# Kernel tuning notes

Hardware: AMD Instinct MI355X
Metric: run time of the kernel (lower is better)

The kernel has to match this reference:

```python
import jax, jax.numpy as jnp
import numpy as np

N = 50000   # nodes
E = 800000  # edges (avg degree 16)
G = 32      # graphs in batch
IN = 128; HID = 64; H = 2; C = 16
NEG_SLOPE = 0.2
BN_EPS = 1e-5


def setup_inputs() -> dict:
    key = jax.random.key(0)
    ks = jax.random.split(key, 16)
    def rn(k, shape, scale=0.1):
        return jax.random.normal(k, shape, jnp.float32) * scale
    return {
        "feat": jax.random.normal(ks[0], (N, IN), jnp.float32),
        "W0": rn(ks[1], (IN, H * HID)),
        "attn0": rn(ks[2], (H, HID)),
        "W1": rn(ks[3], (H * HID, H * HID)),
        "attn1": rn(ks[4], (H, HID)),
        "W2": rn(ks[5], (H * HID, H * HID)),
        "attn2": rn(ks[6], (H, HID)),
        "Wf": rn(ks[7], (H * HID, H * C)),
        "attnf": rn(ks[8], (H, C)),
        "mlp_w1": rn(ks[9], (C, C)),
        "mlp_gamma": jnp.ones((C,), jnp.float32),
        "mlp_beta": jnp.zeros((C,), jnp.float32),
        "mlp_w2": rn(ks[10], (C, C)),
        "src": jax.random.randint(ks[11], (E,), 0, N, jnp.int32),
        "dst": jax.random.randint(ks[12], (E,), 0, N, jnp.int32),
        "node_graph": jnp.sort(jax.random.randint(ks[13], (N,), 0, G, jnp.int32)),
        "num_graphs": G,
    }


def gatv2_layer(h, src, dst, W, attn, act):
    """DGL GATv2Conv with share_weights=True, bias=False, residual=False."""
    n = h.shape[0]
    nh, d = attn.shape
    z = (h @ W).reshape(n, nh, d)                      # [N,H,D]
    zs = z[src]                                        # [E,H,D] gather (src)
    e = jax.nn.leaky_relu(zs + z[dst], NEG_SLOPE)      # [E,H,D]
    score = jnp.einsum('ehd,hd->eh', e, attn)          # [E,H]
    # edge softmax over incoming edges of dst (shift-invariant max trick)
    m = jax.lax.stop_gradient(jax.ops.segment_max(score, dst, num_segments=n))
    a = jnp.exp(score - m[dst])
    denom = jax.ops.segment_sum(a, dst, num_segments=n)[dst]
    alpha = a / jnp.where(denom == 0, 1.0, denom)      # [E,H]
    out = jax.ops.segment_sum(alpha[..., None] * zs, dst, num_segments=n)  # [N,H,D]
    return act(out) if act is not None else out


def reference(feat, W0, attn0, W1, attn1, W2, attn2, Wf, attnf,
              mlp_w1, mlp_gamma, mlp_beta, mlp_w2,
              src, dst, node_graph, num_graphs):
    relu = jax.nn.relu
    n = feat.shape[0]
    h = gatv2_layer(feat, src, dst, W0, attn0, relu).reshape(n, -1)
    h = gatv2_layer(h, src, dst, W1, attn1, relu).reshape(n, -1)
    h = gatv2_layer(h, src, dst, W2, attn2, relu).reshape(n, -1)
    logits = gatv2_layer(h, src, dst, Wf, attnf, None).mean(axis=1)  # [N,C]
    pooled = jax.ops.segment_sum(logits, node_graph, num_segments=num_graphs)  # [G,C]
    # MLP: relu(batchnorm(lin0(x))) -> lin1 (training-mode batch stats, biased var)
    h1 = pooled @ mlp_w1
    mu = h1.mean(axis=0)
    var = h1.var(axis=0)
    h1 = (h1 - mu) / jnp.sqrt(var + BN_EPS) * mlp_gamma + mlp_beta
    out = relu(h1) @ mlp_w2
    return jax.nn.log_softmax(out, axis=-1)
```

## Files before the change

### kernel.cpp

```cpp
#include <hip/hip_runtime.h>
#include <hip/hip_bf16.h>
#include <hip/hip_fp16.h>
#include <math.h>

#define NN 50000
#define EE 800000
#define GG 32
#define HD 64
#define NHEAD 2
#define CCLS 16
#define NEG_SLOPE 0.2f
#define BN_EPS 1e-5f
#define LOG2E 1.4426950408889634f
#define STRIDE 64
#define CURB 6250
#define BUCKCAP 110000
#define SLICES 392
#define LCAP 192

typedef unsigned int u32;
typedef unsigned short u16;
typedef unsigned long long u64;
typedef _Float16 hv2 __attribute__((ext_vector_type(2)));
typedef __fp16   cv2 __attribute__((ext_vector_type(2)));

__device__ __forceinline__ hv2 bch2(u32 u) { union { u32 u; hv2 h; } c; c.u = u; return c.h; }
__device__ __forceinline__ u32 bcu32(hv2 h) { union { hv2 h; u32 u; } c; c.h = h; return c.u; }
__device__ __forceinline__ u32 pkrtz(float a, float b) {
    cv2 r = __builtin_amdgcn_cvt_pkrtz(a, b);
    union { cv2 h; u32 u; } c; c.h = r; return c.u;
}
__device__ __forceinline__ hv2 h2max(hv2 a, hv2 b) {
    return __builtin_elementwise_max(a, b);
}
__device__ __forceinline__ float fdot2(hv2 a, hv2 b, float c) {
#if __has_builtin(__builtin_amdgcn_fdot2)
    union { hv2 h; cv2 c2; } ua, ub;
    ua.h = a; ub.h = b;
    return __builtin_amdgcn_fdot2(ua.c2, ub.c2, c, false);
#else
    return fmaf((float)a[0], (float)b[0], fmaf((float)a[1], (float)b[1], c));
#endif
}
__device__ __forceinline__ int curidx(int d) { return (d & 7) * CURB + (d >> 3); }


__global__ __launch_bounds__(256) void bucket_kernel(const int* __restrict__ src,
                                                     const int* __restrict__ dst,
                                                     int* __restrict__ bcur,
                                                     u32* __restrict__ buckets,
                                                     int* __restrict__ cursor,
                                                     u16* __restrict__ csr_src) {
    __shared__ int cnt[8], base[8];
    __shared__ u32 buf[8 * LCAP];
    int t = threadIdx.x;
    int lane = t & 63;
    if (t < 8) cnt[t] = 0;
    __syncthreads();
    #pragma unroll
    for (int q = 0; q < 4; q++) {
        int e = blockIdx.x * 1024 + q * 256 + t;
        bool v = e < EE;
        int d = v ? dst[e] : 0;
        int s = v ? src[e] : 0;
        int mybucket = v ? (d & 7) : 8;
        u32 pkv = ((u32)d << 16) | (u32)s;
        #pragma unroll
        for (int b = 0; b < 8; b++) {
            u64 m = __ballot(mybucket == b);
            if (m == 0ull) continue;
            int leader = __ffsll((long long)m) - 1;
            int bs = 0;
            if (lane == leader) bs = atomicAdd(&cnt[b], __popcll(m));
            bs = __shfl(bs, leader, 64);
            if (mybucket == b) {
                int pos = bs + __popcll(m & ((1ull << lane) - 1ull));
                if (pos < LCAP) {
                    buf[b * LCAP + pos] = pkv;
                } else {
                    int p = atomicAdd(&cursor[curidx(d)], 1);
                    csr_src[d * STRIDE + p] = (u16)s;
                }
            }
        }
    }
    __syncthreads();
    if (t < 8) {
        int c = min(cnt[t], LCAP);
        cnt[t] = c;
        base[t] = atomicAdd(&bcur[t], c);
    }
    __syncthreads();
    #pragma unroll
    for (int b = 0; b < 8; b++) {
        int c = cnt[b], bs = base[b];
        for (int i = t; i < c; i += 256)
            buckets[b * BUCKCAP + bs + i] = buf[b * LCAP + i];
    }
}


__global__ __launch_bounds__(256) void scatter2_kernel(const u32* __restrict__ buckets,
                                                       const int* __restrict__ bcur,
                                                       int* __restrict__ cursor,
                                                       u16* __restrict__ csr_src) {
    int b = blockIdx.x & 7;
    int slice = blockIdx.x >> 3;
    int cnt = bcur[b];
    const u32* bp = buckets + b * BUCKCAP;
    for (int idx = slice * 256 + threadIdx.x; idx < cnt; idx += SLICES * 256) {
        u32 pk = bp[idx];
        int d = pk >> 16;
        int s = pk & 0xffff;
        int p = atomicAdd(&cursor[b * CURB + (d >> 3)], 1);
        csr_src[d * STRIDE + p] = (u16)s;
    }
}


template<int KOUT, int RPT, bool F16IN>
__device__ __forceinline__ void gemm_body(const void* __restrict__ hv,
                                          const float* __restrict__ W,
                                          u32* __restrict__ z, int n, int blk) {
    constexpr int CT = KOUT / 8;
    constexpr int RT = 256 / CT;
    constexpr int BR = RT * RPT;
    constexpr int WSTR = (KOUT == 128) ? 140 : (KOUT + 4);
    __shared__ __align__(16) u32 WpD[64 * WSTR];
    __shared__ __align__(16) uint4 hsU4[BR * 17];
    int t = threadIdx.x;
    int row0 = blk * BR;

    for (int i = t; i < 64 * (KOUT / 4); i += 256) {
        int k2 = i / (KOUT / 4), cq = i % (KOUT / 4);
        float4 wa = ((const float4*)W)[(2 * k2) * (KOUT / 4) + cq];
        float4 wb = ((const float4*)W)[(2 * k2 + 1) * (KOUT / 4) + cq];
        uint4 d;
        d.x = pkrtz(wa.x, wb.x); d.y = pkrtz(wa.y, wb.y);
        d.z = pkrtz(wa.z, wb.z); d.w = pkrtz(wa.w, wb.w);
        *(uint4*)&WpD[k2 * WSTR + 4 * cq + ((cq >> 3) << 2)] = d;
    }
    for (int i = t; i < BR * 16; i += 256) {
        int r = i >> 4, c16 = i & 15;
        int gr = row0 + r;
        uint4 u = {0, 0, 0, 0};
        if (gr < n) {
            if (F16IN) {
                u = ((const uint4*)hv)[(size_t)gr * 16 + c16];
            } else {
                float4 f0 = ((const float4*)hv)[(size_t)gr * 32 + 2 * c16];
                float4 f1 = ((const float4*)hv)[(size_t)gr * 32 + 2 * c16 + 1];
                u.x = pkrtz(f0.x, f0.y); u.y = pkrtz(f0.z, f0.w);
                u.z = pkrtz(f1.x, f1.y); u.w = pkrtz(f1.z, f1.w);
            }
        }
        hsU4[r * 17 + c16] = u;
    }
    __syncthreads();

    int tc = t % CT, tr = t / CT;
    float acc[RPT][8];
    #pragma unroll
    for (int i = 0; i < RPT; i++)
        #pragma unroll
        for (int c = 0; c < 8; c++) acc[i][c] = 0.f;

    for (int kq = 0; kq < 16; kq++) {
        uint4 a4[RPT];
        #pragma unroll
        for (int i = 0; i < RPT; i++) a4[i] = hsU4[(tr * RPT + i) * 17 + kq];
        #pragma unroll
        for (int j = 0; j < 4; j++) {
            const u32* wrow = &WpD[(4 * kq + j) * WSTR + tc * 8 + ((tc >> 2) << 2)];
            uint4 wa = *(const uint4*)wrow;
            uint4 wb = *(const uint4*)(wrow + 4);
            u32 wd[8] = {wa.x, wa.y, wa.z, wa.w, wb.x, wb.y, wb.z, wb.w};
            #pragma unroll
            for (int i = 0; i < RPT; i++) {
                u32 av[4] = {a4[i].x, a4[i].y, a4[i].z, a4[i].w};
                hv2 a2 = bch2(av[j]);
                #pragma unroll
                for (int c = 0; c < 8; c++)
                    acc[i][c] = fdot2(a2, bch2(wd[c]), acc[i][c]);
            }
        }
    }
    #pragma unroll
    for (int i = 0; i < RPT; i++) {
        int gr = row0 + tr * RPT + i;
        if (gr < n) {
            uint4 p;
            p.x = pkrtz(acc[i][0], acc[i][1]);
            p.y = pkrtz(acc[i][2], acc[i][3]);
            p.z = pkrtz(acc[i][4], acc[i][5]);
            p.w = pkrtz(acc[i][6], acc[i][7]);
            ((uint4*)z)[(size_t)gr * (KOUT / 8) + tc] = p;
        }
    }
}

template<int KOUT, int RPT, bool F16IN>
__global__ __launch_bounds__(256) void gemm_kernel(const void* __restrict__ hv,
                                                   const float* __restrict__ W,
                                                   u32* __restrict__ z, int n) {
    gemm_body<KOUT, RPT, F16IN>(hv, W, z, n, blockIdx.x);
}

__global__ __launch_bounds__(256) void gemm0_kernel(const void* __restrict__ hv,
                                                    const float* __restrict__ W,
                                                    u32* __restrict__ z,
                                                    int* __restrict__ cursor,
                                                    float* __restrict__ pooled) {
    int gid = blockIdx.x * 256 + threadIdx.x;
    if (gid < NN + 8) cursor[gid] = 0;
    if (gid < GG * CCLS) pooled[gid] = 0.f;
    gemm_body<128, 4, false>(hv, W, z, NN, blockIdx.x);
}


__global__ __launch_bounds__(256) void edge_kernel(const u32* __restrict__ z,
                                                   const float* __restrict__ attn,
                                                   const int* __restrict__ cursor,
                                                   const u16* __restrict__ csr_src,
                                                   u32* __restrict__ out, int n) {
    int wave = blockIdx.x * 4 + (threadIdx.x >> 6);
    int lane = threadIdx.x & 63;
    if (wave >= n) return;
    int i = wave;
    int slot = lane >> 3;
    int q8 = lane & 7;
    const uint4* zr = (const uint4*)z;

    size_t rowi = (size_t)i * 16 + q8 * 2;
    uint4 zua = zr[rowi], zub = zr[rowi + 1];
    hv2 zd[8] = {bch2(zua.x), bch2(zua.y), bch2(zua.z), bch2(zua.w),
                 bch2(zub.x), bch2(zub.y), bch2(zub.z), bch2(zub.w)};
    const float4* af = (const float4*)attn;
    float4 a0 = af[q8 * 4 + 0], a1 = af[q8 * 4 + 1];
    float4 a2 = af[q8 * 4 + 2], a3 = af[q8 * 4 + 3];
    hv2 ah[8] = {bch2(pkrtz(a0.x * LOG2E, a0.y * LOG2E)),
                 bch2(pkrtz(a0.z * LOG2E, a0.w * LOG2E)),
                 bch2(pkrtz(a1.x * LOG2E, a1.y * LOG2E)),
                 bch2(pkrtz(a1.z * LOG2E, a1.w * LOG2E)),
                 bch2(pkrtz(a2.x * LOG2E, a2.y * LOG2E)),
                 bch2(pkrtz(a2.z * LOG2E, a2.w * LOG2E)),
                 bch2(pkrtz(a3.x * LOG2E, a3.y * LOG2E)),
                 bch2(pkrtz(a3.z * LOG2E, a3.w * LOG2E))};
    const hv2 slope2 = {(_Float16)NEG_SLOPE, (_Float16)NEG_SLOPE};

    int deg = cursor[curidx(i)];
    const u16* ep = csr_src + i * STRIDE;

    float s = 0.f;
    hv2 acch[8];
    #pragma unroll
    for (int j = 0; j < 8; j++) acch[j] = (hv2){(_Float16)0.f, (_Float16)0.f};

    bool valid = slot < deg;
    int sid = valid ? (int)ep[slot] : i;
    size_t rs = (size_t)sid * 16 + q8 * 2;
    uint4 sa = zr[rs], sb = zr[rs + 1];

    for (int k = 0; k < deg; k += 8) {
        bool more = (k + 8) < deg;
        bool v2 = (k + 8 + slot) < deg;
        uint4 na, nb;
        if (more) {
            int sid2 = v2 ? (int)ep[k + 8 + slot] : i;
            size_t rs2 = (size_t)sid2 * 16 + q8 * 2;
            na = zr[rs2]; nb = zr[rs2 + 1];
        }
        hv2 zs[8] = {bch2(sa.x), bch2(sa.y), bch2(sa.z), bch2(sa.w),
                     bch2(sb.x), bch2(sb.y), bch2(sb.z), bch2(sb.w)};
        float sc = 0.f;
        #pragma unroll
        for (int j = 0; j < 8; j++) {
            hv2 x = zs[j] + zd[j];
            x = h2max(x, x * slope2);
            sc = fdot2(x, ah[j], sc);
        }
        sc += __shfl_xor(sc, 2, 64);
        sc += __shfl_xor(sc, 1, 64);
        float p = valid ? exp2f(sc) : 0.f;
        s += p;
        hv2 p2 = bch2(pkrtz(p, p));
        #pragma unroll
        for (int j = 0; j < 8; j++) acch[j] = p2 * zs[j] + acch[j];
        sa = na; sb = nb; valid = v2;
    }

    #pragma unroll
    for (int off = 8; off <= 32; off <<= 1) {
        s += __shfl_xor(s, off, 64);
        #pragma unroll
        for (int j = 0; j < 8; j++) {
            u32 o = (u32)__shfl_xor((int)bcu32(acch[j]), off, 64);
            acch[j] = acch[j] + bch2(o);
        }
    }

    if (slot == 0) {
        float inv = s > 0.f ? 1.f / s : 0.f;
        hv2 inv2 = bch2(pkrtz(inv, inv));
        const hv2 zero2 = {(_Float16)0.f, (_Float16)0.f};
        uint4 pa, pb;
        pa.x = bcu32(h2max(acch[0] * inv2, zero2));
        pa.y = bcu32(h2max(acch[1] * inv2, zero2));
        pa.z = bcu32(h2max(acch[2] * inv2, zero2));
        pa.w = bcu32(h2max(acch[3] * inv2, zero2));
        pb.x = bcu32(h2max(acch[4] * inv2, zero2));
        pb.y = bcu32(h2max(acch[5] * inv2, zero2));
        pb.z = bcu32(h2max(acch[6] * inv2, zero2));
        pb.w = bcu32(h2max(acch[7] * inv2, zero2));
        ((uint4*)out)[rowi] = pa;
        ((uint4*)out)[rowi + 1] = pb;
    }
}


__global__ __launch_bounds__(256) void edge_final_kernel(const u32* __restrict__ z,
                                                         const float* __restrict__ attn,
                                                         const int* __restrict__ cursor,
                                                         const u16* __restrict__ csr_src,
                                                         const int* __restrict__ node_graph,
                                                         float* __restrict__ pooled, int n) {
    __shared__ float pl[GG * CCLS];
    for (int t = threadIdx.x; t < GG * CCLS; t += 256) pl[t] = 0.f;
    __syncthreads();

    int wave = blockIdx.x * 4 + (threadIdx.x >> 6);
    int lane = threadIdx.x & 63;
    int iv = wave * 2 + (lane >> 5);
    bool mine = iv < n;
    int i = mine ? iv : (n - 1);
    int hl = lane & 31;
    int j = hl >> 3;
    int d8 = hl & 7;
    const uint2* zr = (const uint2*)z;
    uint2 zu = zr[(size_t)i * 8 + d8];
    hv2 zd0 = bch2(zu.x), zd1 = bch2(zu.y);
    float4 av = ((const float4*)attn)[d8];
    hv2 ah0 = bch2(pkrtz(av.x * LOG2E, av.y * LOG2E));
    hv2 ah1 = bch2(pkrtz(av.z * LOG2E, av.w * LOG2E));
    const hv2 slope2 = {(_Float16)NEG_SLOPE, (_Float16)NEG_SLOPE};
    int deg = cursor[curidx(i)];
    const u16* ep = csr_src + i * STRIDE;

    float s = 0.f;
    float accf[4] = {0.f, 0.f, 0.f, 0.f};
    for (int k = 0; k < deg; k += 4) {
        int kk = k + j;
        bool valid = kk < deg;
        int sid = valid ? (int)ep[kk] : i;
        uint2 su = zr[(size_t)sid * 8 + d8];
        hv2 zs0 = bch2(su.x), zs1 = bch2(su.y);
        hv2 x;
        float sc = 0.f;
        x = zs0 + zd0; x = h2max(x, x * slope2); sc = fdot2(x, ah0, sc);
        x = zs1 + zd1; x = h2max(x, x * slope2); sc = fdot2(x, ah1, sc);
        sc += __shfl_xor(sc, 1, 64);
        sc += __shfl_xor(sc, 2, 64);
        float p = valid ? exp2f(sc) : 0.f;
        s += p;
        accf[0] = fmaf(p, (float)zs0[0], accf[0]);
        accf[1] = fmaf(p, (float)zs0[1], accf[1]);
        accf[2] = fmaf(p, (float)zs1[0], accf[2]);
        accf[3] = fmaf(p, (float)zs1[1], accf[3]);
    }
    #pragma unroll
    for (int off = 8; off <= 16; off <<= 1) {
        s += __shfl_xor(s, off, 64);
        #pragma unroll
        for (int jj = 0; jj < 4; jj++) accf[jj] += __shfl_xor(accf[jj], off, 64);
    }
    float inv = s > 0.f ? 1.f / s : 0.f;
    float4 o;
    o.x = accf[0] * inv; o.y = accf[1] * inv; o.z = accf[2] * inv; o.w = accf[3] * inv;
    o.x = 0.5f * (o.x + __shfl_xor(o.x, 4, 64));
    o.y = 0.5f * (o.y + __shfl_xor(o.y, 4, 64));
    o.z = 0.5f * (o.z + __shfl_xor(o.z, 4, 64));
    o.w = 0.5f * (o.w + __shfl_xor(o.w, 4, 64));
    if (mine && j == 0 && (hl & 4) == 0) {
        int g = node_graph[i];
        float* base = &pl[g * 16 + 4 * d8];
        atomicAdd(&base[0], o.x);
        atomicAdd(&base[1], o.y);
        atomicAdd(&base[2], o.z);
        atomicAdd(&base[3], o.w);
    }
    __syncthreads();
    for (int t = threadIdx.x; t < GG * CCLS; t += 256) {
        float v = pl[t];
        if (v != 0.f) atomicAdd(&pooled[t], v);
    }
}


__global__ __launch_bounds__(512) void mlp_kernel(const float* __restrict__ pooled,
                                                  const float* __restrict__ w1,
                                                  const float* __restrict__ gamma,
                                                  const float* __restrict__ beta,
                                                  const float* __restrict__ w2,
                                                  float* __restrict__ out) {
    __shared__ float P[GG * CCLS], H1[GG * CCLS], H2[GG * CCLS], O[GG * CCLS];
    __shared__ float mu[CCLS], rstd[CCLS], rowm[GG], rowl[GG];
    int t = threadIdx.x;
    int r = t >> 4, c = t & 15;
    if (t < GG * CCLS) P[t] = pooled[t];
    __syncthreads();
    if (t < GG * CCLS) {
        float s = 0.f;
        for (int k = 0; k < 16; k++) s += P[r * 16 + k] * w1[k * 16 + c];
        H1[t] = s;
    }
    __syncthreads();
    if (t < CCLS) {
        float s = 0.f;
        for (int rr = 0; rr < GG; rr++) s += H1[rr * 16 + t];
        float mn = s / GG;
        float s2 = 0.f;
        for (int rr = 0; rr < GG; rr++) { float d = H1[rr * 16 + t] - mn; s2 += d * d; }
        mu[t] = mn; rstd[t] = rsqrtf(s2 / GG + BN_EPS);
    }
    __syncthreads();
    if (t < GG * CCLS) {
        float v = (H1[t] - mu[c]) * rstd[c] * gamma[c] + beta[c];
        H2[t] = fmaxf(v, 0.f);
    }
    __syncthreads();
    if (t < GG * CCLS) {
        float s = 0.f;
        for (int k = 0; k < 16; k++) s += H2[r * 16 + k] * w2[k * 16 + c];
        O[t] = s;
    }
    __syncthreads();
    if (t < GG) {
        float mx = -INFINITY;
        for (int k = 0; k < 16; k++) mx = fmaxf(mx, O[t * 16 + k]);
        float l = 0.f;
        for (int k = 0; k < 16; k++) l += __expf(O[t * 16 + k] - mx);
        rowm[t] = mx; rowl[t] = logf(l);
    }
    __syncthreads();
    if (t < GG * CCLS) out[t] = O[t] - rowm[r] - rowl[r];
}


extern "C" void kernel_launch(void* const* d_in, const int* in_sizes, int n_in,
                              void* d_out, int out_size, void* d_ws, size_t ws_size,
                              hipStream_t stream) {
    const float* feat     = (const float*)d_in[0];
    const float* W0       = (const float*)d_in[1];
    const float* attn0    = (const float*)d_in[2];
    const float* W1       = (const float*)d_in[3];
    const float* attn1    = (const float*)d_in[4];
    const float* W2       = (const float*)d_in[5];
    const float* attn2    = (const float*)d_in[6];
    const float* Wf       = (const float*)d_in[7];
    const float* attnf    = (const float*)d_in[8];
    const float* mlp_w1   = (const float*)d_in[9];
    const float* mlp_g    = (const float*)d_in[10];
    const float* mlp_b    = (const float*)d_in[11];
    const float* mlp_w2   = (const float*)d_in[12];
    const int*   src      = (const int*)d_in[13];
    const int*   dst      = (const int*)d_in[14];
    const int*   ngraph   = (const int*)d_in[15];
    float* out = (float*)d_out;

    char* ws = (char*)d_ws;
    size_t off = 0;
    auto alloc = [&](size_t bytes) {
        void* p = ws + off;
        off = (off + bytes + 255) & ~(size_t)255;
        return p;
    };
    u32* z      = (u32*)alloc((size_t)NN * 64 * sizeof(u32));
    u32* hb0    = (u32*)alloc((size_t)NN * 64 * sizeof(u32));
    u32* hb1    = (u32*)alloc((size_t)NN * 64 * sizeof(u32));
    float* pooled = (float*)alloc(GG * CCLS * sizeof(float));
    int* cursor   = (int*)alloc((NN + 8) * sizeof(int));
    int* bcur     = cursor + NN;
    u16* csr_src  = (u16*)alloc((size_t)NN * STRIDE * sizeof(u16));
    u32* buckets  = (u32*)alloc((size_t)8 * BUCKCAP * sizeof(u32));

    int edge_grid = (NN + 3) / 4;
    int edgef_grid = (NN + 7) / 8;
    int gemm_grid = (NN + 63) / 64;
    int buck_grid = (EE + 1023) / 1024;

    gemm0_kernel<<<gemm_grid, 256, 0, stream>>>(feat, W0, z, cursor, pooled);
    bucket_kernel<<<buck_grid, 256, 0, stream>>>(src, dst, bcur, buckets, cursor, csr_src);
    scatter2_kernel<<<8 * SLICES, 256, 0, stream>>>(buckets, bcur, cursor, csr_src);
    edge_kernel<<<edge_grid, 256, 0, stream>>>(z, attn0, cursor, csr_src, hb0, NN);

    gemm_kernel<128, 4, true><<<gemm_grid, 256, 0, stream>>>(hb0, W1, z, NN);
    edge_kernel<<<edge_grid, 256, 0, stream>>>(z, attn1, cursor, csr_src, hb1, NN);

    gemm_kernel<128, 4, true><<<gemm_grid, 256, 0, stream>>>(hb1, W2, z, NN);
    edge_kernel<<<edge_grid, 256, 0, stream>>>(z, attn2, cursor, csr_src, hb0, NN);

    gemm_kernel<32, 1, true><<<gemm_grid, 256, 0, stream>>>(hb0, Wf, z, NN);
    edge_final_kernel<<<edgef_grid, 256, 0, stream>>>(z, attnf, cursor, csr_src,
                                                      ngraph, pooled, NN);

    mlp_kernel<<<1, 512, 0, stream>>>(pooled, mlp_w1, mlp_g, mlp_b, mlp_w2, out);
}
```

Measured before the change: 380.7 us.

## Co-schedule layer-0 GEMM with CSR scatter and fuse MLP into final edge kernel

Moves the layer-0 GEMM out of the first kernel into a combined launch whose blocks either run a K-chunked GEMM tile with a smaller LDS arena or scatter bucketed edges into the CSR, so the two independent jobs share the GPU at the same time. The first kernel is now a small zero-init kernel. The MLP head is folded into the last edge kernel through a last-block-done ticket counter, which removes one launch. The cost is an extra atomic per block and a serial tail in the final block, plus the GEMM reloading W chunks.

```diff
diff --git a/kernel.cpp b/kernel.cpp
--- a/kernel.cpp
+++ b/kernel.cpp
@@ -15,8 +15,13 @@
 #define STRIDE 64
 #define CURB 6250
 #define BUCKCAP 110000
-#define SLICES 392
 #define LCAP 192
+#define NCHUNK ((EE + 1023) / 1024)
+#define NTILE  ((NN + 63) / 64)
+#define G0B 784
+#define SCB 752
+#define NBF (G0B + SCB)
+#define SLC (SCB / 8)
 
 typedef unsigned int u32;
 typedef unsigned short u16;
@@ -43,6 +48,16 @@
 #endif
 }
 __device__ __forceinline__ int curidx(int d) { return (d & 7) * CURB + (d >> 3); }
+
+
+__global__ __launch_bounds__(256) void zero_kernel(int* __restrict__ cursor,
+                                                   float* __restrict__ pooled,
+                                                   int* __restrict__ done) {
+    int g = blockIdx.x * 256 + threadIdx.x;
+    for (int i = g; i < NN + 8; i += gridDim.x * 256) cursor[i] = 0;
+    if (g < GG * CCLS) pooled[g] = 0.f;
+    if (g == 0) *done = 0;
+}
 
 
 __global__ __launch_bounds__(256) void bucket_kernel(const int* __restrict__ src,
@@ -100,24 +115,6 @@
 }
 
 
-__global__ __launch_bounds__(256) void scatter2_kernel(const u32* __restrict__ buckets,
-                                                       const int* __restrict__ bcur,
-                                                       int* __restrict__ cursor,
-                                                       u16* __restrict__ csr_src) {
-    int b = blockIdx.x & 7;
-    int slice = blockIdx.x >> 3;
-    int cnt = bcur[b];
-    const u32* bp = buckets + b * BUCKCAP;
-    for (int idx = slice * 256 + threadIdx.x; idx < cnt; idx += SLICES * 256) {
-        u32 pk = bp[idx];
-        int d = pk >> 16;
-        int s = pk & 0xffff;
-        int p = atomicAdd(&cursor[b * CURB + (d >> 3)], 1);
-        csr_src[d * STRIDE + p] = (u16)s;
-    }
-}
-
-
 template<int KOUT, int RPT, bool F16IN>
 __device__ __forceinline__ void gemm_body(const void* __restrict__ hv,
                                           const float* __restrict__ W,
@@ -206,15 +203,113 @@
     gemm_body<KOUT, RPT, F16IN>(hv, W, z, n, blockIdx.x);
 }
 
-__global__ __launch_bounds__(256) void gemm0_kernel(const void* __restrict__ hv,
-                                                    const float* __restrict__ W,
-                                                    u32* __restrict__ z,
-                                                    int* __restrict__ cursor,
-                                                    float* __restrict__ pooled) {
-    int gid = blockIdx.x * 256 + threadIdx.x;
-    if (gid < NN + 8) cursor[gid] = 0;
-    if (gid < GG * CCLS) pooled[gid] = 0.f;
-    gemm_body<128, 4, false>(hv, W, z, NN, blockIdx.x);
+__device__ __forceinline__ void gemm_body_chunk(const float* __restrict__ hv,
+                                                const float* __restrict__ W,
+                                                u32* __restrict__ z, int n, int blk,
+                                                char* arena) {
+    constexpr int WSTR = 140;
+    constexpr int KC = 16;
+    u32* WpD = (u32*)arena;
+    uint4* hsU4 = (uint4*)(arena + 9216);
+    int t = threadIdx.x;
+    int row0 = blk * 64;
+
+    for (int i = t; i < 64 * 16; i += 256) {
+        int r = i >> 4, c16 = i & 15;
+        int gr = row0 + r;
+        uint4 u = {0, 0, 0, 0};
+        if (gr < n) {
+            float4 f0 = ((const float4*)hv)[(size_t)gr * 32 + 2 * c16];
+            float4 f1 = ((const float4*)hv)[(size_t)gr * 32 + 2 * c16 + 1];
+            u.x = pkrtz(f0.x, f0.y); u.y = pkrtz(f0.z, f0.w);
+            u.z = pkrtz(f1.x, f1.y); u.w = pkrtz(f1.z, f1.w);
+        }
+        hsU4[r * 17 + c16] = u;
+    }
+
+    int tc = t % 16, tr = t / 16;
+    float acc[4][8];
+    #pragma unroll
+    for (int i = 0; i < 4; i++)
+        #pragma unroll
+        for (int c = 0; c < 8; c++) acc[i][c] = 0.f;
+
+    for (int ch = 0; ch < 4; ch++) {
+        __syncthreads();
+        for (int i = t; i < KC * 32; i += 256) {
+            int k2l = i / 32, cq = i % 32;
+            int k2 = ch * KC + k2l;
+            float4 wa = ((const float4*)W)[(2 * k2) * 32 + cq];
+            float4 wb = ((const float4*)W)[(2 * k2 + 1) * 32 + cq];
+            uint4 d;
+            d.x = pkrtz(wa.x, wb.x); d.y = pkrtz(wa.y, wb.y);
+            d.z = pkrtz(wa.z, wb.z); d.w = pkrtz(wa.w, wb.w);
+            *(uint4*)&WpD[k2l * WSTR + 4 * cq + ((cq >> 3) << 2)] = d;
+        }
+        __syncthreads();
+        for (int kqq = 0; kqq < KC / 4; kqq++) {
+            int kq = ch * (KC / 4) + kqq;
+            uint4 a4[4];
+            #pragma unroll
+            for (int i = 0; i < 4; i++) a4[i] = hsU4[(tr * 4 + i) * 17 + kq];
+            #pragma unroll
+            for (int j = 0; j < 4; j++) {
+                const u32* wrow = &WpD[(4 * kqq + j) * WSTR + tc * 8 + ((tc >> 2) << 2)];
+                uint4 wa = *(const uint4*)wrow;
+                uint4 wb = *(const uint4*)(wrow + 4);
+                u32 wd[8] = {wa.x, wa.y, wa.z, wa.w, wb.x, wb.y, wb.z, wb.w};
+                #pragma unroll
+                for (int i = 0; i < 4; i++) {
+                    u32 av[4] = {a4[i].x, a4[i].y, a4[i].z, a4[i].w};
+                    hv2 a2 = bch2(av[j]);
+                    #pragma unroll
+                    for (int c = 0; c < 8; c++)
+                        acc[i][c] = fdot2(a2, bch2(wd[c]), acc[i][c]);
+                }
+            }
+        }
+    }
+    #pragma unroll
+    for (int i = 0; i < 4; i++) {
+        int gr = row0 + tr * 4 + i;
+        if (gr < n) {
+            uint4 p;
+            p.x = pkrtz(acc[i][0], acc[i][1]);
+            p.y = pkrtz(acc[i][2], acc[i][3]);
+            p.z = pkrtz(acc[i][4], acc[i][5]);
+            p.w = pkrtz(acc[i][6], acc[i][7]);
+            ((uint4*)z)[(size_t)gr * 16 + tc] = p;
+        }
+    }
+}
+
+
+__global__ __launch_bounds__(256, 6) void g0scat_kernel(const float* __restrict__ feat,
+                                                        const float* __restrict__ W0,
+                                                        u32* __restrict__ z,
+                                                        const u32* __restrict__ buckets,
+                                                        const int* __restrict__ bcur,
+                                                        int* __restrict__ cursor,
+                                                        u16* __restrict__ csr_src) {
+    __shared__ __align__(16) char arena[26624];
+    int bb = blockIdx.x;
+    if (bb < G0B) {
+        if (bb < NTILE)
+            gemm_body_chunk(feat, W0, z, NN, bb, arena);
+    } else {
+        int sbb = bb - G0B;
+        int b = sbb & 7;
+        int slice = sbb >> 3;
+        int cnt = bcur[b];
+        const u32* bp = buckets + b * BUCKCAP;
+        for (int idx = slice * 256 + threadIdx.x; idx < cnt; idx += SLC * 256) {
+            u32 pk = bp[idx];
+            int d = pk >> 16;
+            int s = pk & 0xffff;
+            int p = atomicAdd(&cursor[curidx(d)], 1);
+            csr_src[d * STRIDE + p] = (u16)s;
+        }
+    }
 }
 
 
@@ -318,13 +413,78 @@
 }
 
 
-__global__ __launch_bounds__(256) void edge_final_kernel(const u32* __restrict__ z,
-                                                         const float* __restrict__ attn,
-                                                         const int* __restrict__ cursor,
-                                                         const u16* __restrict__ csr_src,
-                                                         const int* __restrict__ node_graph,
-                                                         float* __restrict__ pooled, int n) {
-    __shared__ float pl[GG * CCLS];
+__device__ __forceinline__ void mlp_256(const float* __restrict__ pooled,
+                                        const float* __restrict__ w1,
+                                        const float* __restrict__ gamma,
+                                        const float* __restrict__ beta,
+                                        const float* __restrict__ w2,
+                                        float* __restrict__ out, int t, char* arena) {
+    float* P    = (float*)arena;
+    float* H1   = P + 512;
+    float* H2   = H1 + 512;
+    float* O    = H2 + 512;
+    float* mu   = O + 512;
+    float* rstd = mu + 16;
+    float* rowm = rstd + 16;
+    float* rowl = rowm + 32;
+    P[t]       = __hip_atomic_load(&pooled[t], __ATOMIC_RELAXED, __HIP_MEMORY_SCOPE_AGENT);
+    P[t + 256] = __hip_atomic_load(&pooled[t + 256], __ATOMIC_RELAXED, __HIP_MEMORY_SCOPE_AGENT);
+    __syncthreads();
+    for (int e = t; e < 512; e += 256) {
+        int r = e >> 4, c = e & 15;
+        float s = 0.f;
+        for (int k = 0; k < 16; k++) s += P[r * 16 + k] * w1[k * 16 + c];
+        H1[e] = s;
+    }
+    __syncthreads();
+    if (t < CCLS) {
+        float s = 0.f;
+        for (int rr = 0; rr < GG; rr++) s += H1[rr * 16 + t];
+        float mn = s / GG;
+        float s2 = 0.f;
+        for (int rr = 0; rr < GG; rr++) { float d = H1[rr * 16 + t] - mn; s2 += d * d; }
+        mu[t] = mn; rstd[t] = rsqrtf(s2 / GG + BN_EPS);
+    }
+    __syncthreads();
+    for (int e = t; e < 512; e += 256) {
+        int c = e & 15;
+        float v = (H1[e] - mu[c]) * rstd[c] * gamma[c] + beta[c];
+        H2[e] = fmaxf(v, 0.f);
+    }
+    __syncthreads();
+    for (int e = t; e < 512; e += 256) {
+        int r = e >> 4, c = e & 15;
+        float s = 0.f;
+        for (int k = 0; k < 16; k++) s += H2[r * 16 + k] * w2[k * 16 + c];
+        O[e] = s;
+    }
+    __syncthreads();
+    if (t < GG) {
+        float mx = -INFINITY;
+        for (int k = 0; k < 16; k++) mx = fmaxf(mx, O[t * 16 + k]);
+        float l = 0.f;
+        for (int k = 0; k < 16; k++) l += __expf(O[t * 16 + k] - mx);
+        rowm[t] = mx; rowl[t] = logf(l);
+    }
+    __syncthreads();
+    for (int e = t; e < 512; e += 256) out[e] = O[e] - rowm[e >> 4] - rowl[e >> 4];
+}
+
+__global__ __launch_bounds__(256) void edge_final_mlp_kernel(const u32* __restrict__ z,
+                                                             const float* __restrict__ attn,
+                                                             const int* __restrict__ cursor,
+                                                             const u16* __restrict__ csr_src,
+                                                             const int* __restrict__ node_graph,
+                                                             float* __restrict__ pooled, int n,
+                                                             int* __restrict__ done,
+                                                             const float* __restrict__ mlp_w1,
+                                                             const float* __restrict__ mlp_g,
+                                                             const float* __restrict__ mlp_b,
+                                                             const float* __restrict__ mlp_w2,
+                                                             float* __restrict__ out) {
+    __shared__ __align__(16) char arena[8704];
+    __shared__ int lastflag;
+    float* pl = (float*)arena;
     for (int t = threadIdx.x; t < GG * CCLS; t += 256) pl[t] = 0.f;
     __syncthreads();
 
@@ -393,56 +553,17 @@
         float v = pl[t];
         if (v != 0.f) atomicAdd(&pooled[t], v);
     }
-}
-
-
-__global__ __launch_bounds__(512) void mlp_kernel(const float* __restrict__ pooled,
-                                                  const float* __restrict__ w1,
-                                                  const float* __restrict__ gamma,
-                                                  const float* __restrict__ beta,
-                                                  const float* __restrict__ w2,
-                                                  float* __restrict__ out) {
-    __shared__ float P[GG * CCLS], H1[GG * CCLS], H2[GG * CCLS], O[GG * CCLS];
-    __shared__ float mu[CCLS], rstd[CCLS], rowm[GG], rowl[GG];
-    int t = threadIdx.x;
-    int r = t >> 4, c = t & 15;
-    if (t < GG * CCLS) P[t] = pooled[t];
-    __syncthreads();
-    if (t < GG * CCLS) {
-        float s = 0.f;
-        for (int k = 0; k < 16; k++) s += P[r * 16 + k] * w1[k * 16 + c];
-        H1[t] = s;
-    }
-    __syncthreads();
-    if (t < CCLS) {
-        float s = 0.f;
-        for (int rr = 0; rr < GG; rr++) s += H1[rr * 16 + t];
-        float mn = s / GG;
-        float s2 = 0.f;
-        for (int rr = 0; rr < GG; rr++) { float d = H1[rr * 16 + t] - mn; s2 += d * d; }
-        mu[t] = mn; rstd[t] = rsqrtf(s2 / GG + BN_EPS);
-    }
-    __syncthreads();
-    if (t < GG * CCLS) {
-        float v = (H1[t] - mu[c]) * rstd[c] * gamma[c] + beta[c];
-        H2[t] = fmaxf(v, 0.f);
-    }
-    __syncthreads();
-    if (t < GG * CCLS) {
-        float s = 0.f;
-        for (int k = 0; k < 16; k++) s += H2[r * 16 + k] * w2[k * 16 + c];
-        O[t] = s;
-    }
-    __syncthreads();
-    if (t < GG) {
-        float mx = -INFINITY;
-        for (int k = 0; k < 16; k++) mx = fmaxf(mx, O[t * 16 + k]);
-        float l = 0.f;
-        for (int k = 0; k < 16; k++) l += __expf(O[t * 16 + k] - mx);
-        rowm[t] = mx; rowl[t] = logf(l);
-    }
-    __syncthreads();
-    if (t < GG * CCLS) out[t] = O[t] - rowm[r] - rowl[r];
+    __syncthreads();
+    if (threadIdx.x == 0) {
+        int ticket = __hip_atomic_fetch_add(done, 1, __ATOMIC_ACQ_REL,
+                                            __HIP_MEMORY_SCOPE_AGENT);
+        lastflag = (ticket == (int)gridDim.x - 1);
+    }
+    __syncthreads();
+    if (lastflag) {
+        __threadfence();
+        mlp_256(pooled, mlp_w1, mlp_g, mlp_b, mlp_w2, out, threadIdx.x, arena);
+    }
 }
 
 
@@ -482,15 +603,16 @@
     int* bcur     = cursor + NN;
     u16* csr_src  = (u16*)alloc((size_t)NN * STRIDE * sizeof(u16));
     u32* buckets  = (u32*)alloc((size_t)8 * BUCKCAP * sizeof(u32));
+    int* done     = (int*)alloc(256);
 
     int edge_grid = (NN + 3) / 4;
     int edgef_grid = (NN + 7) / 8;
-    int gemm_grid = (NN + 63) / 64;
-    int buck_grid = (EE + 1023) / 1024;
-
-    gemm0_kernel<<<gemm_grid, 256, 0, stream>>>(feat, W0, z, cursor, pooled);
+    int gemm_grid = NTILE;
+    int buck_grid = NCHUNK;
+
+    zero_kernel<<<196, 256, 0, stream>>>(cursor, pooled, done);
     bucket_kernel<<<buck_grid, 256, 0, stream>>>(src, dst, bcur, buckets, cursor, csr_src);
-    scatter2_kernel<<<8 * SLICES, 256, 0, stream>>>(buckets, bcur, cursor, csr_src);
+    g0scat_kernel<<<NBF, 256, 0, stream>>>(feat, W0, z, buckets, bcur, cursor, csr_src);
     edge_kernel<<<edge_grid, 256, 0, stream>>>(z, attn0, cursor, csr_src, hb0, NN);
 
     gemm_kernel<128, 4, true><<<gemm_grid, 256, 0, stream>>>(hb0, W1, z, NN);
@@ -500,8 +622,7 @@
     edge_kernel<<<edge_grid, 256, 0, stream>>>(z, attn2, cursor, csr_src, hb0, NN);
 
     gemm_kernel<32, 1, true><<<gemm_grid, 256, 0, stream>>>(hb0, Wf, z, NN);
-    edge_final_kernel<<<edgef_grid, 256, 0, stream>>>(z, attnf, cursor, csr_src,
-                                                      ngraph, pooled, NN);
-
-    mlp_kernel<<<1, 512, 0, stream>>>(pooled, mlp_w1, mlp_g, mlp_b, mlp_w2, out);
-}
+    edge_final_mlp_kernel<<<edgef_grid, 256, 0, stream>>>(z, attnf, cursor, csr_src,
+                                                          ngraph, pooled, NN, done,
+                                                          mlp_w1, mlp_g, mlp_b, mlp_w2, out);
+}
```

New measurement: 464.2 us. 21.9% more time.
